# Kernel tuning notes

Measured on AMD Instinct MI355X. Metric: run time of the kernel, lower is better.

## Reference

```python
import jax, jax.numpy as jnp
import numpy as np

B, N, D = 2, 128, 512  # batch, tokens, embed_dim (= in_features = out_features)
LAYERS = 3


def setup_inputs() -> dict:
    key = jax.random.key(0)
    ks = jax.random.split(key, 9)
    s = lambda fan_in: 1.0 / np.sqrt(fan_in)
    return {
        "text_embedding": jax.random.normal(ks[0], (B, N, D), dtype=jnp.float32),
        # weights stored as [in, out] so y = x @ W + b (matches torch Linear math)
        "W_rel": jax.random.uniform(ks[1], (2 * D, D), jnp.float32, -s(2 * D), s(2 * D)),
        "b_rel": jax.random.uniform(ks[2], (D,), jnp.float32, -s(2 * D), s(2 * D)),
        "W_go": jax.random.uniform(ks[3], (D, D), jnp.float32, -s(D), s(D)),
        "b_go": jax.random.uniform(ks[4], (D,), jnp.float32, -s(D), s(D)),
        "W_gr": jax.random.uniform(ks[5], (3 * D, D), jnp.float32, -s(3 * D), s(3 * D)),
        "b_gr": jax.random.uniform(ks[6], (D,), jnp.float32, -s(3 * D), s(3 * D)),
        "W_esa": jax.random.uniform(ks[7], (D, D), jnp.float32, -s(D), s(D)),
        "b_esa": jax.random.uniform(ks[8], (D,), jnp.float32, -s(D), s(D)),
    }


def reference(text_embedding, W_rel, b_rel, W_go, b_go, W_gr, b_gr, W_esa, b_esa):
    x = text_embedding  # [B, N, D]
    n = x.shape[1]
    rel = None
    for i in range(LAYERS):
        new_x = jnp.tanh(x @ W_go + b_go)  # [B, N, D]
        # pairwise broadcast-concat: [B, N, N, 2D]
        a = jnp.broadcast_to(x[:, :, None, :], (x.shape[0], n, n, x.shape[-1]))
        b = jnp.broadcast_to(x[:, None, :, :], (x.shape[0], n, n, x.shape[-1]))
        rlf = jnp.concatenate([a, b], axis=3)
        if i == 0:
            rel = rlf @ W_rel + b_rel  # [B, N, N, D]
        rlf2 = jnp.concatenate([rlf, rel], axis=3)  # [B, N, N, 3D]
        rel = jnp.tanh(rlf2 @ W_gr + b_gr)  # [B, N, N, D]
        x = new_x
    rel = rel @ W_esa + b_esa  # [B, N, N, D]
    # original subtracts max over dim=1 then applies Softmax(dim=1); equivalent to stable softmax over axis 1
    attn = jax.nn.softmax(rel, axis=1)
    rel_out = jnp.sum(attn * rel, axis=-2)  # sum over second N axis -> [B, N, D]
    return (x, rel_out)
```

## Files before the change

### kernel.cpp

```cpp
#include <hip/hip_runtime.h>
#include <hip/hip_bf16.h>
#include <stdint.h>


#define DEV static __device__ __forceinline__

typedef float  f32x4   __attribute__((ext_vector_type(4)));
typedef float  f32x16  __attribute__((ext_vector_type(16)));
typedef __bf16 bf16x8  __attribute__((ext_vector_type(8)));
typedef __bf16 bf16x4  __attribute__((ext_vector_type(4)));

DEV float tanh_fast(float x) {
  float e = __expf(2.0f * x);
  return 1.0f - 2.0f * __frcp_rn(e + 1.0f);
}

DEV void gl_lds16(const void* g, void* l) {
  __builtin_amdgcn_global_load_lds(
      (const __attribute__((address_space(1))) unsigned int*)g,
      (__attribute__((address_space(3))) unsigned int*)l, 16, 0, 0);
}

DEV int swz(int row, int kbyte) { return row * 128 + (kbyte ^ ((row & 7) << 4)); }

struct WC { const float* W; __bf16* Wh; __bf16* Wl; };
struct Prep {
  WC w[7];
  const float* x0; __bf16* x0h; __bf16* x0l;
  const float* b_rel; const float* Wgrc; const float* b_gr; float* dvec;
};

__global__ __launch_bounds__(256) void prep_kernel(Prep pp) {
  const int y = blockIdx.y;
  if (y < 7) {
    const WC wc = pp.w[y];
    __shared__ float tile[32][33];
    int t = threadIdx.x;
    int tx = t & 31, ty = t >> 5;
    int bx = blockIdx.x & 15, by = blockIdx.x >> 4;
    int k0 = by * 32, n0 = bx * 32;
#pragma unroll
    for (int r = 0; r < 4; ++r) {
      int k = ty + r * 8;
      tile[k][tx] = wc.W[(size_t)(k0 + k) * 512 + n0 + tx];
    }
    __syncthreads();
#pragma unroll
    for (int r = 0; r < 4; ++r) {
      int n = ty + r * 8;
      float v = tile[tx][n];
      __bf16 h = (__bf16)v;
      wc.Wh[(size_t)(n0 + n) * 512 + k0 + tx] = h;
      wc.Wl[(size_t)(n0 + n) * 512 + k0 + tx] = (__bf16)(v - (float)h);
    }
  } else if (y == 7) {
    int i = blockIdx.x * 256 + threadIdx.x;
    if (i < 32768) {
      float4 v = ((const float4*)pp.x0)[i];
      float vv[4] = {v.x, v.y, v.z, v.w};
      bf16x4 h, l;
#pragma unroll
      for (int e = 0; e < 4; ++e) {
        __bf16 he = (__bf16)vv[e];
        h[e] = he;
        l[e] = (__bf16)(vv[e] - (float)he);
      }
      ((bf16x4*)pp.x0h)[i] = h;
      ((bf16x4*)pp.x0l)[i] = l;
    }
  } else {
    if (blockIdx.x < 2) {
      int n = blockIdx.x * 256 + threadIdx.x;
      float acc = pp.b_gr[n];
#pragma unroll 8
      for (int k = 0; k < 512; ++k) acc += pp.b_rel[k] * pp.Wgrc[(size_t)k * 512 + n];
      pp.dvec[n] = acc;
    }
  }
}

struct MOp {
  const __bf16* Xh; const __bf16* Xl;
  const __bf16* Wh; const __bf16* Wl;
  const float* bias;
  const float* add;
  float* outf;
  __bf16* outh; __bf16* outl;
  int act;
};
struct MBatch { MOp op[5]; };

DEV void mfma_small_body(const MOp& o) {
  const int m0 = ((int)blockIdx.x >> 3) * 64;
  const int n0 = ((int)blockIdx.x & 7) * 64;
  __shared__ __bf16 Ah[64 * 64], Al[64 * 64], Bh[64 * 64], Bl[64 * 64];
  const int t = threadIdx.x, lane = t & 63, wave = t >> 6;
  const int waveM = wave >> 1, waveN = wave & 1;
  const bool comp = (o.Xl != nullptr);

  f32x4 vzero = {0.f, 0.f, 0.f, 0.f};
  f32x4 acc[2][2];
#pragma unroll
  for (int a = 0; a < 2; ++a)
#pragma unroll
    for (int c = 0; c < 2; ++c) acc[a][c] = vzero;

  const int lr = lane >> 3;
  const int lc = ((lane & 7) ^ lr) * 8;

  for (int k0 = 0; k0 < 512; k0 += 64) {
    __syncthreads();
#pragma unroll
    for (int r = 0; r < 2; ++r) {
      const int rb = r * 32 + wave * 8;
      gl_lds16(o.Xh + (size_t)(m0 + rb + lr) * 512 + k0 + lc, &Ah[rb * 64]);
      gl_lds16(o.Wh + (size_t)(n0 + rb + lr) * 512 + k0 + lc, &Bh[rb * 64]);
      if (comp) {
        gl_lds16(o.Xl + (size_t)(m0 + rb + lr) * 512 + k0 + lc, &Al[rb * 64]);
        gl_lds16(o.Wl + (size_t)(n0 + rb + lr) * 512 + k0 + lc, &Bl[rb * 64]);
      }
    }
    __syncthreads();
#pragma unroll
    for (int kk = 0; kk < 2; ++kk) {
      const int kb = kk * 64 + (lane >> 4) * 16;
      const int ml = lane & 15;
      bf16x8 ah[2], bh[2], al[2], bl[2];
#pragma unroll
      for (int tm = 0; tm < 2; ++tm)
        ah[tm] = *(const bf16x8*)((const char*)Ah + swz(waveM * 32 + tm * 16 + ml, kb));
#pragma unroll
      for (int tn = 0; tn < 2; ++tn)
        bh[tn] = *(const bf16x8*)((const char*)Bh + swz(waveN * 32 + tn * 16 + ml, kb));
      if (comp) {
#pragma unroll
        for (int tm = 0; tm < 2; ++tm)
          al[tm] = *(const bf16x8*)((const char*)Al + swz(waveM * 32 + tm * 16 + ml, kb));
#pragma unroll
        for (int tn = 0; tn < 2; ++tn)
          bl[tn] = *(const bf16x8*)((const char*)Bl + swz(waveN * 32 + tn * 16 + ml, kb));
      }
#pragma unroll
      for (int tm = 0; tm < 2; ++tm)
#pragma unroll
        for (int tn = 0; tn < 2; ++tn) {
          acc[tm][tn] = __builtin_amdgcn_mfma_f32_16x16x32_bf16(ah[tm], bh[tn], acc[tm][tn], 0, 0, 0);
          if (comp) {
            acc[tm][tn] = __builtin_amdgcn_mfma_f32_16x16x32_bf16(ah[tm], bl[tn], acc[tm][tn], 0, 0, 0);
            acc[tm][tn] = __builtin_amdgcn_mfma_f32_16x16x32_bf16(al[tm], bh[tn], acc[tm][tn], 0, 0, 0);
          }
        }
    }
  }

  const int quad = lane >> 4, cl = lane & 15;
#pragma unroll
  for (int tm = 0; tm < 2; ++tm) {
#pragma unroll
    for (int r = 0; r < 4; ++r) {
      const int row = m0 + waveM * 32 + tm * 16 + quad * 4 + r;
#pragma unroll
      for (int tn = 0; tn < 2; ++tn) {
        const int col = n0 + waveN * 32 + tn * 16 + cl;
        float v = acc[tm][tn][r];
        if (o.bias) v += o.bias[col];
        if (o.add) v += o.add[(size_t)row * 512 + col];
        if (o.act) v = tanh_fast(v);
        if (o.outf) o.outf[(size_t)row * 512 + col] = v;
        if (o.outh) {
          __bf16 h = (__bf16)v;
          o.outh[(size_t)row * 512 + col] = h;
          o.outl[(size_t)row * 512 + col] = (__bf16)(v - (float)h);
        }
      }
    }
  }
}

__global__ __launch_bounds__(256, 2) void mfma_small_kernel(MBatch batch) {
  mfma_small_body(batch.op[blockIdx.y]);
}

DEV void rel1_unit(const float* __restrict__ A, const float* __restrict__ C,
                   __bf16* __restrict__ R1, size_t u) {
  size_t e = u * 8;
  int d = (int)(e & 511);
  int j = (int)((e >> 9) & 127);
  int bi = (int)(e >> 16);
  int b = bi >> 7;
  const float* ap = &A[(size_t)bi * 512 + d];
  const float* cp = &C[((size_t)(b * 128 + j)) * 512 + d];
  float av[8], cv[8];
  *(float4*)&av[0] = *(const float4*)ap;
  *(float4*)&av[4] = *(const float4*)(ap + 4);
  *(float4*)&cv[0] = *(const float4*)cp;
  *(float4*)&cv[4] = *(const float4*)(cp + 4);
  bf16x8 o;
#pragma unroll
  for (int k = 0; k < 8; ++k) o[k] = (__bf16)tanh_fast(av[k] + cv[k]);
  *(bf16x8*)&R1[e] = o;
}

__global__ __launch_bounds__(256, 2) void m3_rel1_kernel(
    MBatch batch, const float* __restrict__ A, const float* __restrict__ C,
    __bf16* __restrict__ R1) {
  if (blockIdx.y == 3) {
    size_t base = (size_t)blockIdx.x * 256 + threadIdx.x;
#pragma unroll 1
    for (int it = 0; it < 32; ++it)
      rel1_unit(A, C, R1, base + (size_t)it * 65536);
    return;
  }
  if (blockIdx.x >= 32) return;
  mfma_small_body(batch.op[blockIdx.y]);
}

constexpr int BM = 128, BN = 128, BK = 64;

template <int MODE>
__global__ __launch_bounds__(256, 2) void big_gemm_kernel(
    const __bf16* __restrict__ Ab, const __bf16* __restrict__ Wt,
    const float* __restrict__ P, const float* __restrict__ Q,
    const float* __restrict__ bias, __bf16* __restrict__ outb,
    float* __restrict__ outf) {
  __shared__ __bf16 As[BM * BK];
  __shared__ __bf16 Bs[BN * BK];
  const int t = threadIdx.x;
  const int lane = t & 63;
  const int wave = t >> 6;
  const int blk = ((int)blockIdx.x & 7) * 128 + ((int)blockIdx.x >> 3);
  const int bm = blk >> 2;
  const int n0 = (blk & 3) * BN;
  const size_t r0 = (size_t)bm * BM;
  const int b = bm >> 7;
  const int i = bm & 127;
  const int waveM = wave >> 1, waveN = wave & 1;

  const int lr = lane >> 3;
  const int lc = ((lane & 7) ^ lr) * 8;

  f32x16 acc[2][2];
#pragma unroll
  for (int a = 0; a < 2; ++a)
#pragma unroll
    for (int c = 0; c < 2; ++c) acc[a][c] = (f32x16)0.f;

  for (int k0 = 0; k0 < 512; k0 += BK) {
    __syncthreads();
#pragma unroll
    for (int p2 = 0; p2 < 4; ++p2) {
      int rowg = wave * 32 + p2 * 8;
      const __bf16* ga = Ab + (r0 + rowg + lr) * 512 + k0 + lc;
      gl_lds16(ga, &As[rowg * 64]);
      const __bf16* gb = Wt + (size_t)(n0 + rowg + lr) * 512 + k0 + lc;
      gl_lds16(gb, &Bs[rowg * 64]);
    }
    __syncthreads();
    const int ml = lane & 31;
    const int klb = (lane >> 5) * 16;
#pragma unroll
    for (int ks = 0; ks < 4; ++ks) {
      const int kb = ks * 32 + klb;
      bf16x8 af[2], bfr[2];
#pragma unroll
      for (int tm = 0; tm < 2; ++tm)
        af[tm] = *(const bf16x8*)((const char*)As + swz(waveM * 64 + tm * 32 + ml, kb));
#pragma unroll
      for (int tn = 0; tn < 2; ++tn)
        bfr[tn] = *(const bf16x8*)((const char*)Bs + swz(waveN * 64 + tn * 32 + ml, kb));
#pragma unroll
      for (int tm = 0; tm < 2; ++tm)
#pragma unroll
        for (int tn = 0; tn < 2; ++tn)
          acc[tm][tn] = __builtin_amdgcn_mfma_f32_32x32x16_bf16(af[tm], bfr[tn], acc[tm][tn], 0, 0, 0);
    }
  }

  const int cl = lane & 31, lg = lane >> 5;
#pragma unroll
  for (int tm = 0; tm < 2; ++tm) {
#pragma unroll
    for (int tn = 0; tn < 2; ++tn) {
      const int col = n0 + waveN * 64 + tn * 32 + cl;
      float pv;
      if (MODE == 2) pv = bias[col];
      else pv = P[((size_t)(b * 128 + i)) * 512 + col];
#pragma unroll
      for (int reg = 0; reg < 16; ++reg) {
        const int row = waveM * 64 + tm * 32 + (reg & 3) + 8 * (reg >> 2) + 4 * lg;
        float v = acc[tm][tn][reg] + pv;
        if (MODE == 2) {
          outf[(r0 + row) * 512 + col] = v;
        } else {
          v += Q[((size_t)(b * 128 + row)) * 512 + col];
          outb[(r0 + row) * 512 + col] = (__bf16)tanh_fast(v);
        }
      }
    }
  }
}

__global__ __launch_bounds__(256) void softmax_l_kernel(
    const float* __restrict__ S, float* __restrict__ Lb) {
  int idx = blockIdx.x * 256 + threadIdx.x;
  int d = idx & 511;
  int j = (idx >> 9) & 127;
  int b = idx >> 16;
  const float* p = S + ((size_t)b * 16384 + j) * 512 + d;
  float l = 0.f;
#pragma unroll 8
  for (int ii = 0; ii < 128; ++ii) l += __expf(p[(size_t)ii * 65536]);
  Lb[idx] = __frcp_rn(l);
}

__global__ __launch_bounds__(256) void softmax_out_kernel(
    const float* __restrict__ S, const float* __restrict__ Lb,
    float* __restrict__ outp) {
  int idx = blockIdx.x * 256 + threadIdx.x;
  int d = idx & 511;
  int i = (idx >> 9) & 127;
  int b = idx >> 16;
  const float* sp = S + ((size_t)(b * 128 + i)) * 65536 + d;
  const float* lp = Lb + (size_t)b * 65536 + d;
  float acc = 0.f;
#pragma unroll 8
  for (int jj = 0; jj < 128; ++jj) {
    float s = sp[(size_t)jj * 512];
    acc += __expf(s) * lp[(size_t)jj * 512] * s;
  }
  outp[idx] = acc;
}

extern "C" void kernel_launch(void* const* d_in, const int* in_sizes, int n_in,
                              void* d_out, int out_size, void* d_ws, size_t ws_size,
                              hipStream_t stream) {
  const float* x0    = (const float*)d_in[0];
  const float* W_rel = (const float*)d_in[1];
  const float* b_rel = (const float*)d_in[2];
  const float* W_go  = (const float*)d_in[3];
  const float* b_go  = (const float*)d_in[4];
  const float* W_gr  = (const float*)d_in[5];
  const float* b_gr  = (const float*)d_in[6];
  const float* W_esa = (const float*)d_in[7];
  const float* b_esa = (const float*)d_in[8];

  const float* Wrel_top = W_rel;
  const float* Wrel_bot = W_rel + 512 * 512;
  const float* Wgr_a = W_gr;
  const float* Wgr_b = W_gr + 512 * 512;
  const float* Wgr_c = W_gr + 2 * 512 * 512;

  char* ws = (char*)d_ws;
  size_t off = 0;
  auto alloc = [&](size_t bytes) -> void* {
    void* p = ws + off;
    off += (bytes + 255) & ~(size_t)255;
    return p;
  };
  const size_t NREL = 16777216ull;
  float*  S  = (float*)alloc(NREL * 4);
  __bf16* R1 = (__bf16*)alloc(NREL * 2);
  __bf16* R2 = (__bf16*)alloc(NREL * 2);
  float* p0t  = (float*)alloc(131072 * 4);
  float* q0t  = (float*)alloc(131072 * 4);
  float* Abuf = (float*)alloc(131072 * 4);
  float* Cbuf = (float*)alloc(131072 * 4);
  float* p1   = (float*)alloc(131072 * 4);
  float* q1   = (float*)alloc(131072 * 4);
  float* p2   = (float*)alloc(131072 * 4);
  float* q2   = (float*)alloc(131072 * 4);
  float* dvec = (float*)alloc(512 * 4);
  float* Lb   = (float*)alloc(131072 * 4);
  __bf16* x0h = (__bf16*)alloc(131072 * 2);
  __bf16* x0l = (__bf16*)alloc(131072 * 2);
  __bf16* x1h = (__bf16*)alloc(131072 * 2);
  __bf16* x1l = (__bf16*)alloc(131072 * 2);
  __bf16* x2h = (__bf16*)alloc(131072 * 2);
  __bf16* x2l = (__bf16*)alloc(131072 * 2);
  __bf16* u0h = (__bf16*)alloc(131072 * 2);
  __bf16* u0l = (__bf16*)alloc(131072 * 2);
  __bf16* v0h = (__bf16*)alloc(131072 * 2);
  __bf16* v0l = (__bf16*)alloc(131072 * 2);
  __bf16* Wgo_h = (__bf16*)alloc(262144 * 2);
  __bf16* Wgo_l = (__bf16*)alloc(262144 * 2);
  __bf16* Wrt_h = (__bf16*)alloc(262144 * 2);
  __bf16* Wrt_l = (__bf16*)alloc(262144 * 2);
  __bf16* Wrb_h = (__bf16*)alloc(262144 * 2);
  __bf16* Wrb_l = (__bf16*)alloc(262144 * 2);
  __bf16* Wga_h = (__bf16*)alloc(262144 * 2);
  __bf16* Wga_l = (__bf16*)alloc(262144 * 2);
  __bf16* Wgb_h = (__bf16*)alloc(262144 * 2);
  __bf16* Wgb_l = (__bf16*)alloc(262144 * 2);
  __bf16* Wgc_h = (__bf16*)alloc(262144 * 2);
  __bf16* Wgc_l = (__bf16*)alloc(262144 * 2);
  __bf16* Wes_h = (__bf16*)alloc(262144 * 2);
  __bf16* Wes_l = (__bf16*)alloc(262144 * 2);

  float* x3out  = (float*)d_out;
  float* relout = (float*)d_out + 131072;

  Prep pp;
  pp.w[0] = {W_go, Wgo_h, Wgo_l};
  pp.w[1] = {Wrel_top, Wrt_h, Wrt_l};
  pp.w[2] = {Wrel_bot, Wrb_h, Wrb_l};
  pp.w[3] = {Wgr_a, Wga_h, Wga_l};
  pp.w[4] = {Wgr_b, Wgb_h, Wgb_l};
  pp.w[5] = {Wgr_c, Wgc_h, Wgc_l};
  pp.w[6] = {W_esa, Wes_h, Wes_l};
  pp.x0 = x0; pp.x0h = x0h; pp.x0l = x0l;
  pp.b_rel = b_rel; pp.Wgrc = Wgr_c; pp.b_gr = b_gr; pp.dvec = dvec;
  prep_kernel<<<dim3(256, 9), 256, 0, stream>>>(pp);

  MBatch m1 = {};
  m1.op[0] = {x0h, x0l, Wgo_h, Wgo_l, b_go, nullptr, nullptr, x1h, x1l, 1};
  m1.op[1] = {x0h, x0l, Wrt_h, Wrt_l, nullptr, nullptr, nullptr, u0h, u0l, 0};
  m1.op[2] = {x0h, x0l, Wrb_h, Wrb_l, nullptr, nullptr, nullptr, v0h, v0l, 0};
  m1.op[3] = {x0h, x0l, Wga_h, Wga_l, nullptr, nullptr, p0t, nullptr, nullptr, 0};
  m1.op[4] = {x0h, x0l, Wgb_h, Wgb_l, nullptr, nullptr, q0t, nullptr, nullptr, 0};
  mfma_small_kernel<<<dim3(32, 5), 256, 0, stream>>>(m1);

  MBatch m2 = {};
  m2.op[0] = {x1h, x1l, Wgo_h, Wgo_l, b_go, nullptr, nullptr, x2h, x2l, 1};
  m2.op[1] = {u0h, u0l, Wgc_h, Wgc_l, dvec, p0t, Abuf, nullptr, nullptr, 0};
  m2.op[2] = {v0h, v0l, Wgc_h, Wgc_l, nullptr, q0t, Cbuf, nullptr, nullptr, 0};
  m2.op[3] = {x1h, x1l, Wga_h, Wga_l, b_gr, nullptr, p1, nullptr, nullptr, 0};
  m2.op[4] = {x1h, x1l, Wgb_h, Wgb_l, nullptr, nullptr, q1, nullptr, nullptr, 0};
  mfma_small_kernel<<<dim3(32, 5), 256, 0, stream>>>(m2);

  MBatch m3 = {};
  m3.op[0] = {x2h, x2l, Wgo_h, Wgo_l, b_go, nullptr, x3out, nullptr, nullptr, 1};
  m3.op[1] = {x2h, x2l, Wga_h, Wga_l, b_gr, nullptr, p2, nullptr, nullptr, 0};
  m3.op[2] = {x2h, x2l, Wgb_h, Wgb_l, nullptr, nullptr, q2, nullptr, nullptr, 0};
  m3_rel1_kernel<<<dim3(256, 4), 256, 0, stream>>>(m3, Abuf, Cbuf, R1);

  big_gemm_kernel<1><<<1024, 256, 0, stream>>>(R1, Wgc_h, p1, q1, nullptr, R2, nullptr);
  big_gemm_kernel<1><<<1024, 256, 0, stream>>>(R2, Wgc_h, p2, q2, nullptr, R1, nullptr);
  big_gemm_kernel<2><<<1024, 256, 0, stream>>>(R1, Wes_h, nullptr, nullptr, b_esa, nullptr, S);

  softmax_l_kernel<<<512, 256, 0, stream>>>(S, Lb);
  softmax_out_kernel<<<512, 256, 0, stream>>>(S, Lb, relout);
}
```

Measured before the change: 256.0 us.

## Enlarge big GEMM tiles to 256x256 with double-buffered LDS prefetch

The pairwise GEMM kernel moves from 128x128 tiles with 256 threads to 256x256 tiles with 512 threads (8 waves, each computing a 128x64 sub-tile). Operand staging into LDS is now double-buffered, so the next K-slice loads are issued during the current slice's MFMAs, and one barrier per K-step is removed. The aim is more operand reuse per byte loaded and hiding global-to-LDS latency. In exchange it uses 128KB of LDS per block and more accumulator registers, and launches only 256 blocks, which lowers occupancy and the number of blocks available to fill the CUs.

```diff
diff --git a/kernel.cpp b/kernel.cpp
--- a/kernel.cpp
+++ b/kernel.cpp
@@ -215,85 +215,95 @@
   mfma_small_body(batch.op[blockIdx.y]);
 }
 
-constexpr int BM = 128, BN = 128, BK = 64;
 
 template <int MODE>
-__global__ __launch_bounds__(256, 2) void big_gemm_kernel(
+__global__ __launch_bounds__(512, 2) void big_gemm_kernel(
     const __bf16* __restrict__ Ab, const __bf16* __restrict__ Wt,
     const float* __restrict__ P, const float* __restrict__ Q,
     const float* __restrict__ bias, __bf16* __restrict__ outb,
     float* __restrict__ outf) {
-  __shared__ __bf16 As[BM * BK];
-  __shared__ __bf16 Bs[BN * BK];
+  __shared__ __bf16 As[2][256 * 64];
+  __shared__ __bf16 Bs[2][256 * 64];
   const int t = threadIdx.x;
   const int lane = t & 63;
   const int wave = t >> 6;
-  const int blk = ((int)blockIdx.x & 7) * 128 + ((int)blockIdx.x >> 3);
-  const int bm = blk >> 2;
-  const int n0 = (blk & 3) * BN;
-  const size_t r0 = (size_t)bm * BM;
-  const int b = bm >> 7;
-  const int i = bm & 127;
-  const int waveM = wave >> 1, waveN = wave & 1;
+  const int wm = wave >> 2, wn = wave & 3;
+  const int bid = (int)blockIdx.x;
+  const int blk = (bid & 7) * 32 + (bid >> 3);
+  const int bm2 = blk >> 1;
+  const int n0 = (blk & 1) * 256;
+  const size_t r0 = (size_t)bm2 * 256;
+  const int bi0 = bm2 * 2;
 
   const int lr = lane >> 3;
   const int lc = ((lane & 7) ^ lr) * 8;
 
-  f32x16 acc[2][2];
-#pragma unroll
-  for (int a = 0; a < 2; ++a)
+  auto stage2 = [&](int k0, int sel, int p) {
+    const int rowg = wave * 32 + p * 8;
+    gl_lds16(Ab + (r0 + rowg + lr) * 512 + k0 + lc, &As[sel][rowg * 64]);
+    gl_lds16(Wt + (size_t)(n0 + rowg + lr) * 512 + k0 + lc, &Bs[sel][rowg * 64]);
+  };
+
+  f32x16 acc[4][2];
+#pragma unroll
+  for (int a = 0; a < 4; ++a)
 #pragma unroll
     for (int c = 0; c < 2; ++c) acc[a][c] = (f32x16)0.f;
 
-  for (int k0 = 0; k0 < 512; k0 += BK) {
-    __syncthreads();
-#pragma unroll
-    for (int p2 = 0; p2 < 4; ++p2) {
-      int rowg = wave * 32 + p2 * 8;
-      const __bf16* ga = Ab + (r0 + rowg + lr) * 512 + k0 + lc;
-      gl_lds16(ga, &As[rowg * 64]);
-      const __bf16* gb = Wt + (size_t)(n0 + rowg + lr) * 512 + k0 + lc;
-      gl_lds16(gb, &Bs[rowg * 64]);
-    }
-    __syncthreads();
-    const int ml = lane & 31;
-    const int klb = (lane >> 5) * 16;
+#pragma unroll
+  for (int p = 0; p < 4; ++p) stage2(0, 0, p);
+  __syncthreads();
+
+  const int ml = lane & 31;
+  const int klb = (lane >> 5) * 16;
+
+#pragma unroll 1
+  for (int kt = 0; kt < 8; ++kt) {
+    const int sel = kt & 1;
 #pragma unroll
     for (int ks = 0; ks < 4; ++ks) {
+      if (kt < 7 && ks < 2) {
+        stage2((kt + 1) * 64, sel ^ 1, ks * 2);
+        stage2((kt + 1) * 64, sel ^ 1, ks * 2 + 1);
+      }
       const int kb = ks * 32 + klb;
-      bf16x8 af[2], bfr[2];
-#pragma unroll
-      for (int tm = 0; tm < 2; ++tm)
-        af[tm] = *(const bf16x8*)((const char*)As + swz(waveM * 64 + tm * 32 + ml, kb));
+      bf16x8 af[4], bfr[2];
+#pragma unroll
+      for (int tm = 0; tm < 4; ++tm)
+        af[tm] = *(const bf16x8*)((const char*)As[sel] + swz(wm * 128 + tm * 32 + ml, kb));
 #pragma unroll
       for (int tn = 0; tn < 2; ++tn)
-        bfr[tn] = *(const bf16x8*)((const char*)Bs + swz(waveN * 64 + tn * 32 + ml, kb));
-#pragma unroll
-      for (int tm = 0; tm < 2; ++tm)
+        bfr[tn] = *(const bf16x8*)((const char*)Bs[sel] + swz(wn * 64 + tn * 32 + ml, kb));
+#pragma unroll
+      for (int tm = 0; tm < 4; ++tm)
 #pragma unroll
         for (int tn = 0; tn < 2; ++tn)
           acc[tm][tn] = __builtin_amdgcn_mfma_f32_32x32x16_bf16(af[tm], bfr[tn], acc[tm][tn], 0, 0, 0);
     }
+    __syncthreads();
   }
 
   const int cl = lane & 31, lg = lane >> 5;
-#pragma unroll
-  for (int tm = 0; tm < 2; ++tm) {
-#pragma unroll
-    for (int tn = 0; tn < 2; ++tn) {
-      const int col = n0 + waveN * 64 + tn * 32 + cl;
-      float pv;
-      if (MODE == 2) pv = bias[col];
-      else pv = P[((size_t)(b * 128 + i)) * 512 + col];
+  const int bi = bi0 + wm;
+  const int b = bi >> 7;
+#pragma unroll
+  for (int tn = 0; tn < 2; ++tn) {
+    const int col = n0 + wn * 64 + tn * 32 + cl;
+    float pv;
+    if (MODE == 2) pv = bias[col];
+    else pv = P[(size_t)bi * 512 + col];
+#pragma unroll
+    for (int tm = 0; tm < 4; ++tm) {
 #pragma unroll
       for (int reg = 0; reg < 16; ++reg) {
-        const int row = waveM * 64 + tm * 32 + (reg & 3) + 8 * (reg >> 2) + 4 * lg;
+        const int j = tm * 32 + (reg & 3) + 8 * (reg >> 2) + 4 * lg;
+        const size_t grow = r0 + wm * 128 + j;
         float v = acc[tm][tn][reg] + pv;
         if (MODE == 2) {
-          outf[(r0 + row) * 512 + col] = v;
+          outf[grow * 512 + col] = v;
         } else {
-          v += Q[((size_t)(b * 128 + row)) * 512 + col];
-          outb[(r0 + row) * 512 + col] = (__bf16)tanh_fast(v);
+          v += Q[((size_t)(b * 128 + j)) * 512 + col];
+          outb[grow * 512 + col] = (__bf16)tanh_fast(v);
         }
       }
     }
@@ -433,9 +443,9 @@
   m3.op[2] = {x2h, x2l, Wgb_h, Wgb_l, nullptr, nullptr, q2, nullptr, nullptr, 0};
   m3_rel1_kernel<<<dim3(256, 4), 256, 0, stream>>>(m3, Abuf, Cbuf, R1);
 
-  big_gemm_kernel<1><<<1024, 256, 0, stream>>>(R1, Wgc_h, p1, q1, nullptr, R2, nullptr);
-  big_gemm_kernel<1><<<1024, 256, 0, stream>>>(R2, Wgc_h, p2, q2, nullptr, R1, nullptr);
-  big_gemm_kernel<2><<<1024, 256, 0, stream>>>(R1, Wes_h, nullptr, nullptr, b_esa, nullptr, S);
+  big_gemm_kernel<1><<<256, 512, 0, stream>>>(R1, Wgc_h, p1, q1, nullptr, R2, nullptr);
+  big_gemm_kernel<1><<<256, 512, 0, stream>>>(R2, Wgc_h, p2, q2, nullptr, R1, nullptr);
+  big_gemm_kernel<2><<<256, 512, 0, stream>>>(R1, Wes_h, nullptr, nullptr, b_esa, nullptr, S);
 
   softmax_l_kernel<<<512, 256, 0, stream>>>(S, Lb);
   softmax_out_kernel<<<512, 256, 0, stream>>>(S, Lb, relout);
```

After: 341.5 us. 1.33x slower.
